# Kernel optimization log

Hardware: AMD Instinct MI355X
Metric: run time of the kernel (lower is better)

Reference implementation:

```python
import jax, jax.numpy as jnp
import numpy as np
from jax import lax

D_MODEL = 1024
D_STATE = 16
D_CONV = 4
D_INNER = 2 * D_MODEL
BATCH = 2
SEQ = 1024


def setup_inputs() -> dict:
    key = jax.random.key(0)
    ks = jax.random.split(key, 8)
    std = 0.02
    return {
        "x": jax.random.normal(ks[0], (BATCH, SEQ, D_MODEL), jnp.float32),
        "in_proj_w": jax.random.normal(ks[1], (2 * D_INNER, D_MODEL), jnp.float32) * std,
        "conv_w": jax.random.normal(ks[2], (D_INNER, 1, D_CONV), jnp.float32) * 0.1,
        "x_proj_w": jax.random.normal(ks[3], (D_STATE + 1, D_INNER), jnp.float32) * std,
        "dt_w": jax.random.normal(ks[4], (D_INNER, 1), jnp.float32) * std,
        "dt_b": jnp.zeros((D_INNER,), jnp.float32),
        "A_param": jax.random.normal(ks[5], (D_INNER, D_STATE), jnp.float32) * std,
        "D_param": jnp.ones((D_INNER,), jnp.float32),
        "out_w": jax.random.normal(ks[6], (D_MODEL, D_INNER), jnp.float32) * std,
        "out_b": jnp.zeros((D_MODEL,), jnp.float32),
    }


def _silu(v):
    return v * jax.nn.sigmoid(v)


def _mamba_forward(x, in_proj_w, conv_w, x_proj_w, dt_w, dt_b, A_param, D_param, out_w, out_b):
    B, L, _ = x.shape
    # in_proj: [B,L,2*d_inner]
    xz = jnp.einsum('bld,ed->ble', x, in_proj_w)
    u, z = jnp.split(xz, 2, axis=-1)  # each [B,L,d_inner]
    # depthwise causal conv1d along time
    uc = u.transpose(0, 2, 1)  # [B,d_inner,L]
    uc = lax.conv_general_dilated(
        uc, conv_w, window_strides=(1,), padding=[(D_CONV - 1, D_CONV - 1)],
        dimension_numbers=('NCH', 'OIH', 'NCH'), feature_group_count=D_INNER,
    )[:, :, :L]
    u = _silu(uc.transpose(0, 2, 1))  # [B,L,d_inner]
    # x_proj -> (dt scalar, B coeffs)
    x_dbl = jnp.einsum('bld,ed->ble', u, x_proj_w)  # [B,L,d_state+1]
    dt_in = x_dbl[..., :1]                          # [B,L,1]
    Bmat = x_dbl[..., 1:]                           # [B,L,d_state]
    delta = jax.nn.softplus(dt_in * dt_w[:, 0] + dt_b)  # [B,L,d_inner]
    A = -jnp.exp(A_param)                            # [d_inner,d_state]

    # selective scan (time-major lax.scan)
    def step(h, inp):
        d_t, b_t = inp  # [B,d_inner], [B,d_state]
        h = jnp.exp(A * d_t[..., None]) * h + d_t[..., None] * b_t[:, None, :]
        y = jnp.einsum('bdn,bn->bd', h, b_t)
        return h, y

    h0 = jnp.zeros((B, D_INNER, D_STATE), x.dtype)
    _, ys = lax.scan(step, h0, (delta.transpose(1, 0, 2), Bmat.transpose(1, 0, 2)))
    y = ys.transpose(1, 0, 2) + u * D_param  # [B,L,d_inner]
    y = y * _silu(z)
    return jnp.einsum('bld,ed->ble', y, out_w) + out_b


def reference(x, in_proj_w, conv_w, x_proj_w, dt_w, dt_b, A_param, D_param, out_w, out_b):
    return _mamba_forward(x, in_proj_w, conv_w, x_proj_w, dt_w, dt_b, A_param, D_param, out_w, out_b)
```

## Files before the change

kernel.cpp:

```cpp
#include <hip/hip_runtime.h>
#include <stdint.h>
#include <stddef.h>

#define D_MODEL 1024
#define D_STATE 16
#define D_INNER 2048
#define BATCH   2
#define SEQ     1024
#define MROWS   (BATCH*SEQ)

#define NCH 32
#define TCH (SEQ/NCH)
#define NREC (BATCH*D_INNER*D_STATE)

#define XKS 8
#define XKC (D_INNER/XKS)

typedef __bf16 bf16x8 __attribute__((ext_vector_type(8)));
typedef float  f32x4  __attribute__((ext_vector_type(4)));

__device__ __forceinline__ unsigned short f2bf(float f) {
    unsigned int u = __float_as_uint(f);
    u += 0x7fffu + ((u >> 16) & 1u);
    return (unsigned short)(u >> 16);
}
__device__ __forceinline__ float bf2f(unsigned short v) {
    return __uint_as_float((unsigned int)v << 16);
}

__device__ __forceinline__ void gl_lds16(const unsigned short* g, unsigned short* l) {
    __builtin_amdgcn_global_load_lds(
        (const __attribute__((address_space(1))) unsigned int*)g,
        (__attribute__((address_space(3))) unsigned int*)l, 16, 0, 0);
}

__global__ void cvt_all_kernel(const float* __restrict__ x,
                               const float* __restrict__ w1,
                               const float* __restrict__ w2,
                               const float* __restrict__ xw,
                               unsigned short* __restrict__ xb,
                               unsigned short* __restrict__ wbi,
                               unsigned short* __restrict__ wbo,
                               unsigned short* __restrict__ wbp) {
    int blk = blockIdx.x, tid = threadIdx.x;
    if (blk < 8192) {
        const float* src; unsigned short* dst; int i;
        if (blk < 2048)      { src = x;  dst = xb;  i = blk * 1024 + tid * 4; }
        else if (blk < 6144) { src = w1; dst = wbi; i = (blk - 2048) * 1024 + tid * 4; }
        else                 { src = w2; dst = wbo; i = (blk - 6144) * 1024 + tid * 4; }
        float4 v = *(const float4*)(src + i);
        ushort4 o;
        o.x = f2bf(v.x); o.y = f2bf(v.y); o.z = f2bf(v.z); o.w = f2bf(v.w);
        *(ushort4*)(dst + i) = o;
    } else {
        int id = (blk - 8192) * 256 + tid;
        wbp[id] = (id < 17 * D_INNER) ? f2bf(xw[id]) : (unsigned short)0;
    }
}

template<int NT, bool SPLITK2, bool OUT_BF16>
__global__ void gemm_bf16_kernel(const unsigned short* __restrict__ A,
                                 const unsigned short* __restrict__ Bw,
                                 void* __restrict__ Cv,
                                 int M, int N, int K) {
    constexpr int NTW = NT / 32;
    constexpr int BCH = NT / 8;
    __shared__ __align__(16) unsigned short Al[2 * 128 * 32];
    __shared__ __align__(16) unsigned short Bl[2 * NT * 32];

    const int tid  = threadIdx.x;
    const int lane = tid & 63;
    const int wid  = tid >> 6;
    const int wm   = wid >> 1;
    const int wn   = wid & 1;
    const int ln   = lane & 15;
    const int q    = lane >> 4;
    const int mblk = blockIdx.y * 128;
    const int nblk = blockIdx.x * NT;
    const int srow = lane >> 2;
    const int spart = lane & 3;

    const int kbeg = SPLITK2 ? blockIdx.z * (K / 2) : 0;
    const int kend = SPLITK2 ? kbeg + K / 2 : K;

    f32x4 acc[4][NTW] = {};

    for (int k0 = kbeg; k0 < kend; k0 += 64) {
        #pragma unroll
        for (int h = 0; h < 4; ++h) {
            int j = wid * 4 + h;
            int kh = j & 1, rb = j >> 1;
            int row = rb * 16 + srow;
            gl_lds16(A + (size_t)(mblk + row) * K + k0 + kh * 32 + spart * 8,
                     Al + kh * 4096 + rb * 512);
        }
        #pragma unroll
        for (int h = 0; h < BCH / 4; ++h) {
            int j = wid * (BCH / 4) + h;
            int kh = j & 1, rb = j >> 1;
            int row = rb * 16 + srow;
            gl_lds16(Bw + (size_t)(nblk + row) * K + k0 + kh * 32 + spart * 8,
                     Bl + kh * (NT * 32) + rb * 512);
        }
        __syncthreads();

        #pragma unroll
        for (int kh = 0; kh < 2; ++kh) {
            bf16x8 af[4], bfr[NTW];
            #pragma unroll
            for (int mt = 0; mt < 4; ++mt)
                af[mt] = *(const bf16x8*)(Al + kh * 4096 + (wm * 64 + mt * 16 + ln) * 32 + q * 8);
            #pragma unroll
            for (int nt = 0; nt < NTW; ++nt)
                bfr[nt] = *(const bf16x8*)(Bl + kh * (NT * 32) + (wn * (NT/2) + nt * 16 + ln) * 32 + q * 8);
            #pragma unroll
            for (int mt = 0; mt < 4; ++mt)
                #pragma unroll
                for (int nt = 0; nt < NTW; ++nt)
                    acc[mt][nt] = __builtin_amdgcn_mfma_f32_16x16x32_bf16(
                        af[mt], bfr[nt], acc[mt][nt], 0, 0, 0);
        }
        __syncthreads();
    }

    size_t cofs = SPLITK2 ? (size_t)blockIdx.z * M * N : 0;
    #pragma unroll
    for (int mt = 0; mt < 4; ++mt) {
        #pragma unroll
        for (int nt = 0; nt < NTW; ++nt) {
            int col = nblk + wn * (NT/2) + nt * 16 + ln;
            #pragma unroll
            for (int r = 0; r < 4; ++r) {
                int row = mblk + wm * 64 + mt * 16 + q * 4 + r;
                if (OUT_BF16)
                    ((unsigned short*)Cv)[cofs + (size_t)row * N + col] = f2bf(acc[mt][nt][r]);
                else
                    ((float*)Cv)[cofs + (size_t)row * N + col] = acc[mt][nt][r];
            }
        }
    }
}

__global__ void splitk_reduce_kernel(const float* __restrict__ part,
                                     const float* __restrict__ bias,
                                     float* __restrict__ out) {
    int i = (blockIdx.x * 256 + threadIdx.x) * 4;
    int n = i & (D_MODEL - 1);
    float4 a = *(const float4*)(part + i);
    float4 b = *(const float4*)(part + (size_t)MROWS * D_MODEL + i);
    float4 bv = *(const float4*)(bias + n);
    float4 o;
    o.x = a.x + b.x + bv.x; o.y = a.y + b.y + bv.y;
    o.z = a.z + b.z + bv.z; o.w = a.w + b.w + bv.w;
    *(float4*)(out + i) = o;
}

__global__ void conv_silu_kernel(const unsigned short* __restrict__ xzb,
                                 const float* __restrict__ conv_w,
                                 unsigned short* __restrict__ ub) {
    int idx = blockIdx.x * blockDim.x + threadIdx.x;
    int d = idx & (D_INNER - 1);
    int m = idx >> 11;
    int l = m & (SEQ - 1);
    const float* w = conv_w + d * 4;
    float s = 0.f;
    #pragma unroll
    for (int j = 0; j < 4; ++j) {
        if (l - j >= 0) s += w[3 - j] * bf2f(xzb[(size_t)(m - j) * 4096 + d]);
    }
    float sig = 1.f / (1.f + __expf(-s));
    ub[idx] = f2bf(s * sig);
}

__global__ void xproj_mfma_kernel(const unsigned short* __restrict__ ub,
                                  const unsigned short* __restrict__ wbp,
                                  float* __restrict__ part) {
    __shared__ __align__(16) unsigned short Al[64 * 64];
    __shared__ __align__(16) unsigned short Bl[32 * 64];

    const int tid  = threadIdx.x;
    const int lane = tid & 63;
    const int wid  = tid >> 6;
    const int ln   = lane & 15;
    const int q    = lane >> 4;
    const int m0   = blockIdx.y * 64;
    const int ks   = blockIdx.x;
    const int srow = lane >> 3;
    const int spart = lane & 7;

    f32x4 acc[2] = {};

    for (int it = 0; it < 4; ++it) {
        int k0 = ks * XKC + it * 64;
        #pragma unroll
        for (int h = 0; h < 2; ++h) {
            int j = wid * 2 + h;
            int row = j * 8 + srow;
            gl_lds16(ub + (size_t)(m0 + row) * D_INNER + k0 + spart * 8, Al + j * 512);
        }
        {
            int row = wid * 8 + srow;
            gl_lds16(wbp + (size_t)row * D_INNER + k0 + spart * 8, Bl + wid * 512);
        }
        __syncthreads();

        bf16x8 af[2], bfr[2][2];
        #pragma unroll
        for (int kh = 0; kh < 2; ++kh) {
            af[kh] = *(const bf16x8*)(Al + (wid * 16 + ln) * 64 + kh * 32 + q * 8);
            bfr[0][kh] = *(const bf16x8*)(Bl + (0 * 16 + ln) * 64 + kh * 32 + q * 8);
            bfr[1][kh] = *(const bf16x8*)(Bl + (1 * 16 + ln) * 64 + kh * 32 + q * 8);
        }
        #pragma unroll
        for (int kh = 0; kh < 2; ++kh) {
            acc[0] = __builtin_amdgcn_mfma_f32_16x16x32_bf16(af[kh], bfr[0][kh], acc[0], 0, 0, 0);
            acc[1] = __builtin_amdgcn_mfma_f32_16x16x32_bf16(af[kh], bfr[1][kh], acc[1], 0, 0, 0);
        }
        __syncthreads();
    }

    #pragma unroll
    for (int nf = 0; nf < 2; ++nf) {
        #pragma unroll
        for (int r = 0; r < 4; ++r) {
            int m = m0 + wid * 16 + q * 4 + r;
            part[((size_t)ks * MROWS + m) * 32 + nf * 16 + ln] = acc[nf][r];
        }
    }
}

__global__ void xproj_reduce_kernel(const float* __restrict__ part,
                                    float* __restrict__ dti,
                                    float* __restrict__ Bm) {
    int id = blockIdx.x * 256 + threadIdx.x;
    int m = id >> 5, n = id & 31;
    float s = 0.f;
    #pragma unroll
    for (int ks = 0; ks < XKS; ++ks) s += part[(size_t)ks * MROWS * 32 + id];
    if (n == 0) dti[m] = s;
    else if (n < 17) Bm[(size_t)m * D_STATE + (n - 1)] = s;
}

__device__ __forceinline__ float softplus_f(float xv) {
    return fmaxf(xv, 0.f) + __logf(1.f + __expf(-fabsf(xv)));
}

__global__ void scanA_kernel(const float* __restrict__ dt_in,
                             const float* __restrict__ Bm,
                             const float* __restrict__ dt_w,
                             const float* __restrict__ dt_b,
                             const float* __restrict__ A_param,
                             float* __restrict__ Pg,
                             float* __restrict__ Sg) {
    __shared__ float sdt[TCH];
    __shared__ float sB[TCH * D_STATE];
    const int tid = threadIdx.x;
    const int b = blockIdx.z, c = blockIdx.y;
    const int d = blockIdx.x * 256 + tid;

    if (tid < TCH) sdt[tid] = dt_in[b * SEQ + c * TCH + tid];
    if (tid < TCH * D_STATE / 4)
        ((float4*)sB)[tid] = ((const float4*)(Bm + ((size_t)(b * SEQ + c * TCH)) * D_STATE))[tid];
    __syncthreads();

    const float dtw = dt_w[d], dtb = dt_b[d];
    float aA[D_STATE], h[D_STATE];
    #pragma unroll
    for (int n4 = 0; n4 < 4; ++n4) {
        float4 ap = ((const float4*)(A_param + (size_t)d * D_STATE))[n4];
        aA[n4*4+0] = -__expf(ap.x); aA[n4*4+1] = -__expf(ap.y);
        aA[n4*4+2] = -__expf(ap.z); aA[n4*4+3] = -__expf(ap.w);
    }
    #pragma unroll
    for (int n = 0; n < D_STATE; ++n) h[n] = 0.f;
    float tsum = 0.f;

    for (int t = 0; t < TCH; ++t) {
        float sp = softplus_f(sdt[t] * dtw + dtb);
        tsum += sp;
        #pragma unroll
        for (int n = 0; n < D_STATE; ++n) {
            float a = __expf(aA[n] * sp);
            h[n] = a * h[n] + sp * sB[t * D_STATE + n];
        }
    }

    size_t base = (size_t)c * NREC + ((size_t)(b * D_INNER + d)) * D_STATE;
    #pragma unroll
    for (int n4 = 0; n4 < 4; ++n4) {
        float4 pv, sv;
        pv.x = __expf(aA[n4*4+0] * tsum); pv.y = __expf(aA[n4*4+1] * tsum);
        pv.z = __expf(aA[n4*4+2] * tsum); pv.w = __expf(aA[n4*4+3] * tsum);
        sv.x = h[n4*4+0]; sv.y = h[n4*4+1]; sv.z = h[n4*4+2]; sv.w = h[n4*4+3];
        *(float4*)(Pg + base + n4 * 4) = pv;
        *(float4*)(Sg + base + n4 * 4) = sv;
    }
}

__global__ void scanB_kernel(const float* __restrict__ Pg,
                             const float* __restrict__ Sg,
                             float* __restrict__ Hin) {
    int idx = blockIdx.x * 256 + threadIdx.x;
    float h = 0.f;
    #pragma unroll
    for (int c = 0; c < NCH; ++c) {
        size_t o = (size_t)c * NREC + idx;
        Hin[o] = h;
        h = Pg[o] * h + Sg[o];
    }
}

__global__ void scanC_kernel(const float* __restrict__ dt_in,
                             const float* __restrict__ Bm,
                             const float* __restrict__ dt_w,
                             const float* __restrict__ dt_b,
                             const float* __restrict__ A_param,
                             const float* __restrict__ Hin,
                             const unsigned short* __restrict__ ub,
                             const unsigned short* __restrict__ xzb,
                             const float* __restrict__ Dp,
                             unsigned short* __restrict__ ypb) {
    __shared__ float sdt[TCH];
    __shared__ float sB[TCH * D_STATE];
    const int tid = threadIdx.x;
    const int b = blockIdx.z, c = blockIdx.y;
    const int d = blockIdx.x * 256 + tid;

    if (tid < TCH) sdt[tid] = dt_in[b * SEQ + c * TCH + tid];
    if (tid < TCH * D_STATE / 4)
        ((float4*)sB)[tid] = ((const float4*)(Bm + ((size_t)(b * SEQ + c * TCH)) * D_STATE))[tid];
    __syncthreads();

    const float dtw = dt_w[d], dtb = dt_b[d];
    const float Dv = Dp[d];
    float aA[D_STATE], h[D_STATE];
    #pragma unroll
    for (int n4 = 0; n4 < 4; ++n4) {
        float4 ap = ((const float4*)(A_param + (size_t)d * D_STATE))[n4];
        aA[n4*4+0] = -__expf(ap.x); aA[n4*4+1] = -__expf(ap.y);
        aA[n4*4+2] = -__expf(ap.z); aA[n4*4+3] = -__expf(ap.w);
    }
    size_t hbase = (size_t)c * NREC + ((size_t)(b * D_INNER + d)) * D_STATE;
    #pragma unroll
    for (int n4 = 0; n4 < 4; ++n4) {
        float4 hv = *(const float4*)(Hin + hbase + n4 * 4);
        h[n4*4+0] = hv.x; h[n4*4+1] = hv.y; h[n4*4+2] = hv.z; h[n4*4+3] = hv.w;
    }

    const size_t mrow0 = (size_t)b * SEQ + c * TCH;
    for (int t = 0; t < TCH; ++t) {
        float sp = softplus_f(sdt[t] * dtw + dtb);
        float y0 = 0.f, y1 = 0.f, y2 = 0.f, y3 = 0.f;
        #pragma unroll
        for (int n4 = 0; n4 < 4; ++n4) {
            #pragma unroll
            for (int j = 0; j < 4; ++j) {
                int n = n4 * 4 + j;
                float Bv = sB[t * D_STATE + n];
                float a = __expf(aA[n] * sp);
                h[n] = a * h[n] + sp * Bv;
                float p = h[n] * Bv;
                if (n4 == 0) y0 += p; else if (n4 == 1) y1 += p;
                else if (n4 == 2) y2 += p; else y3 += p;
            }
        }
        float y = (y0 + y1) + (y2 + y3);
        size_t m = mrow0 + t;
        float z  = bf2f(xzb[m * 4096 + D_INNER + d]);
        float sz = z / (1.f + __expf(-z));
        float uv = bf2f(ub[m * D_INNER + d]);
        ypb[m * D_INNER + d] = f2bf((y + uv * Dv) * sz);
    }
}

extern "C" void kernel_launch(void* const* d_in, const int* in_sizes, int n_in,
                              void* d_out, int out_size, void* d_ws, size_t ws_size,
                              hipStream_t stream) {
    const float* x         = (const float*)d_in[0];
    const float* in_proj_w = (const float*)d_in[1];
    const float* conv_w    = (const float*)d_in[2];
    const float* x_proj_w  = (const float*)d_in[3];
    const float* dt_w      = (const float*)d_in[4];
    const float* dt_b      = (const float*)d_in[5];
    const float* A_param   = (const float*)d_in[6];
    const float* D_param   = (const float*)d_in[7];
    const float* out_w     = (const float*)d_in[8];
    const float* out_b     = (const float*)d_in[9];
    float* out = (float*)d_out;

    char* ws = (char*)d_ws;
    unsigned short* xb  = (unsigned short*)(ws);
    unsigned short* wbi = (unsigned short*)(ws + (4u  << 20));
    unsigned short* wbo = (unsigned short*)(ws + (12u << 20));
    unsigned short* xzb = (unsigned short*)(ws + (16u << 20));
    unsigned short* ub  = (unsigned short*)(ws + (32u << 20));
    float*          dti = (float*)(ws + (40u << 20));
    float*          Bm  = (float*)(ws + (40u << 20) + (64u  << 10));
    unsigned short* wbp = (unsigned short*)(ws + (40u << 20) + (192u << 10));
    float*          xpt = (float*)(ws + (40u << 20) + (512u << 10));
    float*          Pg  = (float*)(ws + (44u << 20));
    float*          Sg  = (float*)(ws + (52u << 20));
    float*          Hin = (float*)(ws + (60u << 20));
    unsigned short* ypb = (unsigned short*)(ws + (68u << 20));
    float*          g2p = (float*)(ws + (76u << 20));

    cvt_all_kernel<<<dim3(8448), 256, 0, stream>>>(
        x, in_proj_w, out_w, x_proj_w, xb, wbi, wbo, wbp);

    gemm_bf16_kernel<128, false, true><<<dim3(4096 / 128, MROWS / 128), 256, 0, stream>>>(
        xb, wbi, xzb, MROWS, 2 * D_INNER, D_MODEL);

    conv_silu_kernel<<<dim3(MROWS * D_INNER / 256), 256, 0, stream>>>(xzb, conv_w, ub);

    xproj_mfma_kernel<<<dim3(XKS, MROWS / 64), 256, 0, stream>>>(ub, wbp, xpt);
    xproj_reduce_kernel<<<dim3(MROWS * 32 / 256), 256, 0, stream>>>(xpt, dti, Bm);

    scanA_kernel<<<dim3(D_INNER / 256, NCH, BATCH), 256, 0, stream>>>(
        dti, Bm, dt_w, dt_b, A_param, Pg, Sg);
    scanB_kernel<<<dim3(NREC / 256), 256, 0, stream>>>(Pg, Sg, Hin);
    scanC_kernel<<<dim3(D_INNER / 256, NCH, BATCH), 256, 0, stream>>>(
        dti, Bm, dt_w, dt_b, A_param, Hin, ub, xzb, D_param, ypb);

    gemm_bf16_kernel<64, true, false><<<dim3(1024 / 64, MROWS / 128, 2), 256, 0, stream>>>(
        ypb, wbo, g2p, MROWS, D_MODEL, D_INNER);

    splitk_reduce_kernel<<<dim3(MROWS * D_MODEL / 1024), 256, 0, stream>>>(g2p, out_b, out);
}
```

Baseline: 220.7 us.

## Double-buffer LDS staging in GEMM and x_proj kernels, vectorize conv+SiLU

After: 220.2 us. Within noise of the previous version (-0.2%).

```diff
diff --git a/kernel.cpp b/kernel.cpp
--- a/kernel.cpp
+++ b/kernel.cpp
@@ -18,6 +18,7 @@
 
 typedef __bf16 bf16x8 __attribute__((ext_vector_type(8)));
 typedef float  f32x4  __attribute__((ext_vector_type(4)));
+typedef unsigned short u16x8 __attribute__((ext_vector_type(8)));
 
 __device__ __forceinline__ unsigned short f2bf(float f) {
     unsigned int u = __float_as_uint(f);
@@ -65,8 +66,8 @@
                                  int M, int N, int K) {
     constexpr int NTW = NT / 32;
     constexpr int BCH = NT / 8;
-    __shared__ __align__(16) unsigned short Al[2 * 128 * 32];
-    __shared__ __align__(16) unsigned short Bl[2 * NT * 32];
+    __shared__ __align__(16) unsigned short Al[2][2 * 128 * 32];
+    __shared__ __align__(16) unsigned short Bl[2][2 * NT * 32];
 
     const int tid  = threadIdx.x;
     const int lane = tid & 63;
@@ -85,14 +86,14 @@
 
     f32x4 acc[4][NTW] = {};
 
-    for (int k0 = kbeg; k0 < kend; k0 += 64) {
+    auto stage = [&](int buf, int k0) {
         #pragma unroll
         for (int h = 0; h < 4; ++h) {
             int j = wid * 4 + h;
             int kh = j & 1, rb = j >> 1;
             int row = rb * 16 + srow;
             gl_lds16(A + (size_t)(mblk + row) * K + k0 + kh * 32 + spart * 8,
-                     Al + kh * 4096 + rb * 512);
+                     Al[buf] + kh * 4096 + rb * 512);
         }
         #pragma unroll
         for (int h = 0; h < BCH / 4; ++h) {
@@ -100,19 +101,26 @@
             int kh = j & 1, rb = j >> 1;
             int row = rb * 16 + srow;
             gl_lds16(Bw + (size_t)(nblk + row) * K + k0 + kh * 32 + spart * 8,
-                     Bl + kh * (NT * 32) + rb * 512);
-        }
-        __syncthreads();
+                     Bl[buf] + kh * (NT * 32) + rb * 512);
+        }
+    };
+
+    stage(0, kbeg);
+    __syncthreads();
+    int cur = 0;
+
+    for (int k0 = kbeg; k0 < kend; k0 += 64) {
+        if (k0 + 64 < kend) stage(cur ^ 1, k0 + 64);
 
         #pragma unroll
         for (int kh = 0; kh < 2; ++kh) {
             bf16x8 af[4], bfr[NTW];
             #pragma unroll
             for (int mt = 0; mt < 4; ++mt)
-                af[mt] = *(const bf16x8*)(Al + kh * 4096 + (wm * 64 + mt * 16 + ln) * 32 + q * 8);
+                af[mt] = *(const bf16x8*)(Al[cur] + kh * 4096 + (wm * 64 + mt * 16 + ln) * 32 + q * 8);
             #pragma unroll
             for (int nt = 0; nt < NTW; ++nt)
-                bfr[nt] = *(const bf16x8*)(Bl + kh * (NT * 32) + (wn * (NT/2) + nt * 16 + ln) * 32 + q * 8);
+                bfr[nt] = *(const bf16x8*)(Bl[cur] + kh * (NT * 32) + (wn * (NT/2) + nt * 16 + ln) * 32 + q * 8);
             #pragma unroll
             for (int mt = 0; mt < 4; ++mt)
                 #pragma unroll
@@ -121,6 +129,7 @@
                         af[mt], bfr[nt], acc[mt][nt], 0, 0, 0);
         }
         __syncthreads();
+        cur ^= 1;
     }
 
     size_t cofs = SPLITK2 ? (size_t)blockIdx.z * M * N : 0;
@@ -158,25 +167,42 @@
 __global__ void conv_silu_kernel(const unsigned short* __restrict__ xzb,
                                  const float* __restrict__ conv_w,
                                  unsigned short* __restrict__ ub) {
-    int idx = blockIdx.x * blockDim.x + threadIdx.x;
-    int d = idx & (D_INNER - 1);
-    int m = idx >> 11;
+    int idx = blockIdx.x * 256 + threadIdx.x;
+    int d8 = idx & 255;
+    int m = idx >> 8;
     int l = m & (SEQ - 1);
-    const float* w = conv_w + d * 4;
-    float s = 0.f;
+    int d = d8 * 8;
+    const float4* wv = (const float4*)(conv_w + (size_t)d * 4);
+    float4 w[8];
+    #pragma unroll
+    for (int e = 0; e < 8; ++e) w[e] = wv[e];
+    float s[8] = {0.f, 0.f, 0.f, 0.f, 0.f, 0.f, 0.f, 0.f};
     #pragma unroll
     for (int j = 0; j < 4; ++j) {
-        if (l - j >= 0) s += w[3 - j] * bf2f(xzb[(size_t)(m - j) * 4096 + d]);
-    }
-    float sig = 1.f / (1.f + __expf(-s));
-    ub[idx] = f2bf(s * sig);
+        if (l - j >= 0) {
+            u16x8 r = *(const u16x8*)(xzb + (size_t)(m - j) * 4096 + d);
+            #pragma unroll
+            for (int e = 0; e < 8; ++e) {
+                float wt = (j == 0) ? w[e].w : (j == 1) ? w[e].z
+                         : (j == 2) ? w[e].y : w[e].x;
+                s[e] += wt * bf2f(r[e]);
+            }
+        }
+    }
+    u16x8 o;
+    #pragma unroll
+    for (int e = 0; e < 8; ++e) {
+        float sig = 1.f / (1.f + __expf(-s[e]));
+        o[e] = f2bf(s[e] * sig);
+    }
+    *(u16x8*)(ub + (size_t)m * D_INNER + d) = o;
 }
 
 __global__ void xproj_mfma_kernel(const unsigned short* __restrict__ ub,
                                   const unsigned short* __restrict__ wbp,
                                   float* __restrict__ part) {
-    __shared__ __align__(16) unsigned short Al[64 * 64];
-    __shared__ __align__(16) unsigned short Bl[32 * 64];
+    __shared__ __align__(16) unsigned short Al[2][64 * 64];
+    __shared__ __align__(16) unsigned short Bl[2][32 * 64];
 
     const int tid  = threadIdx.x;
     const int lane = tid & 63;
@@ -190,26 +216,33 @@
 
     f32x4 acc[2] = {};
 
-    for (int it = 0; it < 4; ++it) {
+    auto stage = [&](int buf, int it) {
         int k0 = ks * XKC + it * 64;
         #pragma unroll
         for (int h = 0; h < 2; ++h) {
             int j = wid * 2 + h;
             int row = j * 8 + srow;
-            gl_lds16(ub + (size_t)(m0 + row) * D_INNER + k0 + spart * 8, Al + j * 512);
+            gl_lds16(ub + (size_t)(m0 + row) * D_INNER + k0 + spart * 8, Al[buf] + j * 512);
         }
         {
             int row = wid * 8 + srow;
-            gl_lds16(wbp + (size_t)row * D_INNER + k0 + spart * 8, Bl + wid * 512);
-        }
-        __syncthreads();
+            gl_lds16(wbp + (size_t)row * D_INNER + k0 + spart * 8, Bl[buf] + wid * 512);
+        }
+    };
+
+    stage(0, 0);
+    __syncthreads();
+    int cur = 0;
+
+    for (int it = 0; it < 4; ++it) {
+        if (it < 3) stage(cur ^ 1, it + 1);
 
         bf16x8 af[2], bfr[2][2];
         #pragma unroll
         for (int kh = 0; kh < 2; ++kh) {
-            af[kh] = *(const bf16x8*)(Al + (wid * 16 + ln) * 64 + kh * 32 + q * 8);
-            bfr[0][kh] = *(const bf16x8*)(Bl + (0 * 16 + ln) * 64 + kh * 32 + q * 8);
-            bfr[1][kh] = *(const bf16x8*)(Bl + (1 * 16 + ln) * 64 + kh * 32 + q * 8);
+            af[kh] = *(const bf16x8*)(Al[cur] + (wid * 16 + ln) * 64 + kh * 32 + q * 8);
+            bfr[0][kh] = *(const bf16x8*)(Bl[cur] + (0 * 16 + ln) * 64 + kh * 32 + q * 8);
+            bfr[1][kh] = *(const bf16x8*)(Bl[cur] + (1 * 16 + ln) * 64 + kh * 32 + q * 8);
         }
         #pragma unroll
         for (int kh = 0; kh < 2; ++kh) {
@@ -217,6 +250,7 @@
             acc[1] = __builtin_amdgcn_mfma_f32_16x16x32_bf16(af[kh], bfr[1][kh], acc[1], 0, 0, 0);
         }
         __syncthreads();
+        cur ^= 1;
     }
 
     #pragma unroll
@@ -410,7 +444,7 @@
     gemm_bf16_kernel<128, false, true><<<dim3(4096 / 128, MROWS / 128), 256, 0, stream>>>(
         xb, wbi, xzb, MROWS, 2 * D_INNER, D_MODEL);
 
-    conv_silu_kernel<<<dim3(MROWS * D_INNER / 256), 256, 0, stream>>>(xzb, conv_w, ub);
+    conv_silu_kernel<<<dim3(MROWS), 256, 0, stream>>>(xzb, conv_w, ub);
 
     xproj_mfma_kernel<<<dim3(XKS, MROWS / 64), 256, 0, stream>>>(ub, wbp, xpt);
     xproj_reduce_kernel<<<dim3(MROWS * 32 / 256), 256, 0, stream>>>(xpt, dti, Bm);
```
